# Kernel optimization log

Measured on AMD Instinct MI355X. Metric: run time of the kernel, lower is better.

Reference implementation:

```python
import jax, jax.numpy as jnp
import numpy as np

G, T, P, M = 512, 25, 10, 5
E = 32          # config.embedding_size
D0 = 2 * E      # initial node embedding dim (h_0)
HID = 32        # signed SAGE output dim
H = 128         # lstm_hidden_size
NE = 40         # edges per vote-graph per sign
N = G * T * P   # total nodes across all vote graphs
LSTM_IN = 2 * HID + 2  # 66


def _seg_mean(vals, idx, n):
    s = jax.ops.segment_sum(vals, idx, num_segments=n)
    c = jax.ops.segment_sum(jnp.ones((idx.shape[0], 1), vals.dtype), idx, num_segments=n)
    return s / jnp.maximum(c, 1.0)


def _l2norm(x, eps=1e-12):
    return x / jnp.maximum(jnp.linalg.norm(x, axis=-1, keepdims=True), eps)


def _globalize(local):
    # local: [G, T, NE] player ids in [0, P) -> flat global node ids in [0, N)
    off = (jnp.arange(G * T, dtype=local.dtype) * P).reshape(G, T, 1)
    return (local + off).reshape(-1)


def _forward(x0, add_info, Wb_pos, bb_pos, Wb_neg, bb_neg,
             Wd_pos, bd_pos, Wd_neg, bd_neg,
             W_ih, W_hh, b_ih, b_hh, hx0, cx0, Wf, bf,
             pos_src, pos_dst, neg_src, neg_dst):
    x = x0.reshape(N, D0)
    pr, pc = _globalize(pos_src), _globalize(pos_dst)
    nr, nc = _globalize(neg_src), _globalize(neg_dst)

    # base signed SAGE: cat(mean of neighbors, self) @ W + b, l2-normalized
    hp = _l2norm(jnp.concatenate([_seg_mean(x[pc], pr, N), x], -1) @ Wb_pos + bb_pos)
    hn = _l2norm(jnp.concatenate([_seg_mean(x[nc], nr, N), x], -1) @ Wb_neg + bb_neg)

    for l in range(2):  # layer_num - 1 deep layers
        app_in = _seg_mean(hp[pc], pr, N)
        app_out = _seg_mean(hp[pr], pc, N)
        ann_in = _seg_mean(hn[nc], nr, N)
        ann_out = _seg_mean(hn[nr], nc, N)
        anp_in = _seg_mean(hn[pc], pr, N)  # neg embeddings over pos edges
        apn_in = _seg_mean(hp[nc], nr, N)  # pos embeddings over neg edges
        feats_p = jnp.concatenate([app_in, app_out, ann_in, ann_out, anp_in, hp, hn], -1)
        feats_n = jnp.concatenate([ann_in, ann_out, app_in, app_out, apn_in, hn, hp], -1)
        hp_new = _l2norm(feats_p @ Wd_pos[l] + bd_pos[l])
        hn = _l2norm(feats_n @ Wd_neg[l] + bd_neg[l])
        hp = hp_new

    # per-vote embedding: cat(h_pos, h_neg, add_info)
    emb = jnp.concatenate([hp, hn], -1).reshape(G, T, P, 2 * HID)
    add_rep = jnp.repeat(add_info, T // M, axis=1)   # [G, T, P, 2]
    seq = jnp.concatenate([emb, add_rep], -1)         # [G, T, P, 66]
    seq = seq.transpose(1, 0, 2, 3).reshape(T, G * P, LSTM_IN)

    # one distinct LSTMCell per timestep (cell_num = 25)
    def step(carry, inp):
        h, c = carry
        x_t, wih, whh, bih, bhh = inp
        gates = x_t @ wih.T + bih + h @ whh.T + bhh
        i, f, g, o = jnp.split(gates, 4, axis=-1)
        c = jax.nn.sigmoid(f) * c + jax.nn.sigmoid(i) * jnp.tanh(g)
        h = jax.nn.sigmoid(o) * jnp.tanh(c)
        return (h, c), None

    (h_last, _), _ = jax.lax.scan(
        step, (hx0.reshape(G * P, H), cx0.reshape(G * P, H)),
        (seq, W_ih, W_hh, b_ih, b_hh))
    return (h_last @ Wf + bf).reshape(G, P, E)


def setup_inputs() -> dict:
    key = jax.random.key(0)
    ks = jax.random.split(key, 24)
    s = 0.1  # weight scale to keep activations/gates in a sane range
    return {
        "x0": jax.random.normal(ks[0], (G, T, P, D0), jnp.float32),
        "add_info": jax.random.uniform(ks[1], (G, M, P, 2), jnp.float32),
        "Wb_pos": jax.random.normal(ks[2], (2 * D0, HID), jnp.float32) * s,
        "bb_pos": jnp.zeros((HID,), jnp.float32),
        "Wb_neg": jax.random.normal(ks[3], (2 * D0, HID), jnp.float32) * s,
        "bb_neg": jnp.zeros((HID,), jnp.float32),
        "Wd_pos": jax.random.normal(ks[4], (2, 7 * HID, HID), jnp.float32) * s,
        "bd_pos": jnp.zeros((2, HID), jnp.float32),
        "Wd_neg": jax.random.normal(ks[5], (2, 7 * HID, HID), jnp.float32) * s,
        "bd_neg": jnp.zeros((2, HID), jnp.float32),
        "W_ih": jax.random.normal(ks[6], (T, 4 * H, LSTM_IN), jnp.float32) * s,
        "W_hh": jax.random.normal(ks[7], (T, 4 * H, H), jnp.float32) * s,
        "b_ih": jnp.zeros((T, 4 * H), jnp.float32),
        "b_hh": jnp.zeros((T, 4 * H), jnp.float32),
        "hx0": jax.random.uniform(ks[8], (G, P, H), jnp.float32),
        "cx0": jax.random.uniform(ks[9], (G, P, H), jnp.float32),
        "Wf": jax.random.normal(ks[10], (H, E), jnp.float32) * s,
        "bf": jnp.zeros((E,), jnp.float32),
        "pos_src": jax.random.randint(ks[11], (G, T, NE), 0, P, jnp.int32),
        "pos_dst": jax.random.randint(ks[12], (G, T, NE), 0, P, jnp.int32),
        "neg_src": jax.random.randint(ks[13], (G, T, NE), 0, P, jnp.int32),
        "neg_dst": jax.random.randint(ks[14], (G, T, NE), 0, P, jnp.int32),
    }


def reference(x0, add_info, Wb_pos, bb_pos, Wb_neg, bb_neg, Wd_pos, bd_pos,
              Wd_neg, bd_neg, W_ih, W_hh, b_ih, b_hh, hx0, cx0, Wf, bf,
              pos_src, pos_dst, neg_src, neg_dst):
    return _forward(x0, add_info, Wb_pos, bb_pos, Wb_neg, bb_neg,
                    Wd_pos, bd_pos, Wd_neg, bd_neg,
                    W_ih, W_hh, b_ih, b_hh, hx0, cx0, Wf, bf,
                    pos_src, pos_dst, neg_src, neg_dst)
```

## Files before the change

### kernel.cpp

```cpp
#include <hip/hip_runtime.h>
#include <math.h>

#define GG 512
#define TT 25
#define PP 10
#define MM 5
#define EE 32
#define HID 32
#define HH 128
#define NEDGE 40
#define NGRAPH (GG*TT)
#define NTOT (GG*TT*PP)

typedef __attribute__((ext_vector_type(8))) short short8v;
typedef __attribute__((ext_vector_type(4))) short short4v;
typedef __attribute__((ext_vector_type(4))) float f32x4;

#define AIDX(s,ki,mt,l) (((((s)*6+(ki))*2+(mt))*64+(l))*8)
#define WB_PER_T 196608

#define AXI(sp,mt,ki) ((((sp)*5+(mt))*2+(ki))*512)
#define AHI(sp,wh,mt) ((((sp)*2+(wh))*5+(mt))*512)
#define NWG 73728

#define MFMA16(a,b,c) __builtin_amdgcn_mfma_f32_16x16x32_bf16(a,b,c,0,0,0)

__device__ __forceinline__ unsigned short f2bf(float x){
    unsigned u = __float_as_uint(x);
    u += 0x7fffu + ((u >> 16) & 1u);
    return (unsigned short)(u >> 16);
}
__device__ __forceinline__ float bf2f(unsigned short s){
    return __uint_as_float(((unsigned)s) << 16);
}
__device__ __forceinline__ float sigm(float x){ return 1.f/(1.f+__expf(-x)); }
__device__ __forceinline__ float tanh_fast(float x){
    float ax = fabsf(x);
    float e  = __expf(-2.f*ax);
    float t  = (1.f-e)/(1.f+e);
    return copysignf(t, x);
}

__global__ void prep_kernel(const float* __restrict__ W_ih, const float* __restrict__ W_hh,
                            const float* __restrict__ b_ih, const float* __restrict__ b_hh,
                            const float* __restrict__ Wb_pos, const float* __restrict__ Wb_neg,
                            const float* __restrict__ Wd_pos, const float* __restrict__ Wd_neg,
                            short* __restrict__ wB, float* __restrict__ wadd,
                            float* __restrict__ bsum, short* __restrict__ wG)
{
    const int NW = TT*WB_PER_T;
    const int NA = TT*2*512;
    const int NB = TT*512;
    const int total = NW + NA + NB + NWG;
    for (int idx = blockIdx.x*blockDim.x + threadIdx.x; idx < total;
         idx += gridDim.x*blockDim.x) {
        if (idx < NW) {
            int e  = idx & 7;
            int l  = (idx >> 3) & 63;
            int nt = (idx >> 9) & 31;
            int rest = idx >> 14;
            int ki = rest % 6; rest /= 6;
            int s  = rest & 1;
            int t  = rest >> 1;
            int k  = ki*32 + (l >> 4)*8 + e;
            int n  = nt*16 + (l & 15);
            float wv = (k < 128) ? W_hh[(size_t)(t*512 + n)*128 + k]
                                 : W_ih[(size_t)(t*512 + n)*66 + (k - 128)];
            unsigned short hi = f2bf(wv);
            unsigned short outv = (s == 0) ? hi : f2bf(wv - bf2f(hi));
            wB[idx] = (short)outv;
        } else if (idx < NW + NA) {
            int i2 = idx - NW;
            int t = i2 / 1024, r = i2 % 1024;
            int cc = r >> 9, n = r & 511;
            wadd[i2] = W_ih[(size_t)(t*512 + n)*66 + 64 + cc];
        } else if (idx < NW + NA + NB) {
            int i3 = idx - NW - NA;
            bsum[i3] = b_ih[i3] + b_hh[i3];
        } else {
            int i4 = idx - NW - NA - NB;
            int e  = i4 & 7;
            int ll = (i4 >> 3) & 63;
            int nt = (i4 >> 9) & 1;
            int sp = (i4 >> 10) & 1;
            int u  = i4 >> 11;
            int n  = nt*16 + (ll & 15);
            int krow = (ll >> 4)*8 + e;
            float wv;
            if (u < 8) {
                int sgn = u >> 2, prod = (u >> 1) & 1, ki = u & 1;
                const float* Wb = sgn ? Wb_neg : Wb_pos;
                wv = Wb[(prod*64 + ki*32 + krow)*32 + n];
            } else {
                int v = u - 8;
                int wid = v % 7, sgn = (v / 7) & 1, lyr = v / 14;
                const float* Wd = (sgn ? Wd_neg : Wd_pos) + lyr*7168;
                wv = Wd[(wid*32 + krow)*32 + n];
            }
            unsigned short hi = f2bf(wv);
            wG[i4] = (sp == 0) ? (short)hi : (short)f2bf(wv - bf2f(hi));
        }
    }
}

__global__ __launch_bounds__(256) void graph_kernel(
    const float* __restrict__ x0,
    const float* __restrict__ bb_pos, const float* __restrict__ bb_neg,
    const float* __restrict__ bd_pos, const float* __restrict__ bd_neg,
    const short* __restrict__ wG,
    const int* __restrict__ pos_src, const int* __restrict__ pos_dst,
    const int* __restrict__ neg_src, const int* __restrict__ neg_dst,
    float* __restrict__ emb)
{
    __shared__ short U[10240];
    __shared__ float Yf[5760];
    __shared__ float Adj[8][4][10][10];

    const int tid = threadIdx.x;
    const int w   = tid >> 6;
    const int l   = tid & 63;
    const int li  = l & 15;
    const int lk  = l >> 4;
    const int s   = tid >> 7;
    const int rg  = (tid >> 3) & 15;
    const int c4  = tid & 7;
    const int gq  = rg >> 1;
    const int nbase = (rg & 1)*5;

    for (int i = tid; i < 1280; i += 256) {
        int row = i >> 4, kq = i & 15;
        float4 f = ((const float4*)x0)[(size_t)blockIdx.x*1280 + i];
        int k0 = kq*4;
        int ln = (row & 15) + 16*((k0 >> 3) & 3);
        int ki = k0 >> 5, e0 = k0 & 7, mt = row >> 4;
        float vv[4] = {f.x, f.y, f.z, f.w};
        short4v hi4, lo4;
#pragma unroll
        for (int e2 = 0; e2 < 4; ++e2) {
            unsigned short h2 = f2bf(vv[e2]);
            hi4[e2] = (short)h2;
            lo4[e2] = (short)f2bf(vv[e2] - bf2f(h2));
        }
        *(short4v*)&U[AXI(0,mt,ki) + ln*8 + e0] = hi4;
        *(short4v*)&U[AXI(1,mt,ki) + ln*8 + e0] = lo4;
    }

    int*   Ses  = (int*)Yf;
    float* Cm   = Yf + 1280;
    float* Scnt = Yf + 2880;
    for (int i = tid; i < 1280; i += 256) {
        int g = i / 160, r = i % 160, b = r / 40, e = r % 40;
        const int* p = (b==0)?pos_src:(b==1)?pos_dst:(b==2)?neg_src:neg_dst;
        Ses[i] = p[(blockIdx.x*8 + g)*40 + e];
    }
    for (int i = tid; i < 1600; i += 256) Cm[i] = 0.f;
    __syncthreads();
    for (int i = tid; i < 640; i += 256) {
        int g = i / 80, r = i % 80, si = r / 40, e = r % 40;
        int src = Ses[g*160 + (2*si)*40 + e];
        int dst = Ses[g*160 + (2*si+1)*40 + e];
        atomicAdd(&Cm[(g*2 + si)*100 + src*10 + dst], 1.f);
    }
    __syncthreads();
    for (int i = tid; i < 320; i += 256) {
        int g = i / 40, r = i % 40, b = r / 10, n = r % 10;
        int si = b >> 1, isCol = b & 1;
        float ssum = 0.f;
        for (int m = 0; m < 10; ++m)
            ssum += isCol ? Cm[(g*2+si)*100 + m*10 + n] : Cm[(g*2+si)*100 + n*10 + m];
        Scnt[i] = fmaxf(ssum, 1.f);
    }
    __syncthreads();
    for (int i = tid; i < 3200; i += 256) {
        int g = i / 400, r = i % 400, a = r / 100, rr = r % 100;
        int n = rr / 10, m = rr % 10;
        int si = a >> 1, isOut = a & 1;
        float cv = isOut ? Cm[(g*2+si)*100 + m*10 + n] : Cm[(g*2+si)*100 + n*10 + m];
        Adj[g][a][n][m] = cv / Scnt[g*40 + a*10 + n];
    }
    __syncthreads();

    f32x4 acc2[5];

    {
        const float* bb = s ? bb_neg : bb_pos;
        f32x4 b4 = *(const f32x4*)(bb + c4*4);
#pragma unroll
        for (int jj = 0; jj < 5; ++jj) acc2[jj] = b4;
    }
    for (int prod = 0; prod < 2; ++prod) {
        for (int i = 0; i < 5; ++i) {
            int jid = w*5 + i;
            int sgn = (jid >= 10);
            int rem = jid - 10*sgn;
            int nt  = (rem >= 5);
            int mt2 = rem - 5*nt;
            f32x4 cf = {0.f, 0.f, 0.f, 0.f};
            for (int ki = 0; ki < 2; ++ki) {
                short8v ah = *(const short8v*)&U[AXI(0,mt2,ki) + l*8];
                short8v al = *(const short8v*)&U[AXI(1,mt2,ki) + l*8];
                int u = sgn*4 + prod*2 + ki;
                const short* wp = wG + ((((size_t)u*2 + 0)*2 + nt)*64 + l)*8;
                short8v bh = *(const short8v*)wp;
                short8v bl = *(const short8v*)(wp + 1024);
                cf = MFMA16(ah, bh, cf);
                cf = MFMA16(ah, bl, cf);
                cf = MFMA16(al, bh, cf);
            }
#pragma unroll
            for (int r = 0; r < 4; ++r)
                Yf[(sgn*80 + mt2*16 + lk*4 + r)*36 + nt*16 + li] = cf[r];
        }
        __syncthreads();
        if (prod == 0) {
            int a = 2*s;
            for (int m = 0; m < 10; ++m) {
                f32x4 y = *(const f32x4*)&Yf[(s*80 + gq*10 + m)*36 + c4*4];
#pragma unroll
                for (int jj = 0; jj < 5; ++jj)
                    acc2[jj] += Adj[gq][a][nbase+jj][m] * y;
            }
        } else {
#pragma unroll
            for (int jj = 0; jj < 5; ++jj)
                acc2[jj] += *(const f32x4*)&Yf[(s*80 + rg*5 + jj)*36 + c4*4];
        }
        __syncthreads();
    }
#pragma unroll
    for (int jj = 0; jj < 5; ++jj) {
        f32x4 v = acc2[jj];
        float ss = v[0]*v[0] + v[1]*v[1] + v[2]*v[2] + v[3]*v[3];
        ss += __shfl_xor(ss,1); ss += __shfl_xor(ss,2); ss += __shfl_xor(ss,4);
        float rn = 1.f / fmaxf(sqrtf(ss), 1e-12f);
        v *= rn;
        int row = rg*5 + jj;
        int mt2 = row >> 4;
        int k0 = c4*4;
        int ln = (row & 15) + 16*((k0 >> 3) & 3);
        float vv[4] = {v[0], v[1], v[2], v[3]};
        short4v hi4, lo4;
#pragma unroll
        for (int e2 = 0; e2 < 4; ++e2) {
            unsigned short h2 = f2bf(vv[e2]);
            hi4[e2] = (short)h2;
            lo4[e2] = (short)f2bf(vv[e2] - bf2f(h2));
        }
        *(short4v*)&U[AHI(0,s,mt2) + ln*8 + (k0 & 7)] = hi4;
        *(short4v*)&U[AHI(1,s,mt2) + ln*8 + (k0 & 7)] = lo4;
    }
    __syncthreads();

    for (int lyr = 0; lyr < 2; ++lyr) {
        {
            const float* bd = (s ? bd_neg : bd_pos) + lyr*32;
            f32x4 b4 = *(const f32x4*)(bd + c4*4);
#pragma unroll
            for (int jj = 0; jj < 5; ++jj) acc2[jj] = b4;
        }
        for (int b = 0; b < 5; ++b) {
            const int np   = (b == 0 || b == 4) ? 2 : 1;
            const int rel0 = (b == 2 || b == 3) ? 1 : 0;
            const int wid0 = (b == 4) ? 5 : b;
            for (int i = 0; i < 5; ++i) {
                int jid = w*5 + i;
                int sgn = (jid >= 10);
                int rem = jid - 10*sgn;
                int nt  = (rem >= 5);
                int mt2 = rem - 5*nt;
                f32x4 cf = {0.f, 0.f, 0.f, 0.f};
                {
                    int wh = sgn ^ rel0;
                    int u = 8 + (lyr*2 + sgn)*7 + wid0;
                    short8v ah = *(const short8v*)&U[AHI(0,wh,mt2) + l*8];
                    short8v al = *(const short8v*)&U[AHI(1,wh,mt2) + l*8];
                    const short* wp = wG + ((((size_t)u*2 + 0)*2 + nt)*64 + l)*8;
                    short8v bh = *(const short8v*)wp;
                    short8v bl = *(const short8v*)(wp + 1024);
                    cf = MFMA16(ah, bh, cf);
                    cf = MFMA16(ah, bl, cf);
                    cf = MFMA16(al, bh, cf);
                }
                if (np == 2) {
                    int wid1 = (b == 0) ? 4 : 6;
                    int wh = sgn ^ 1;
                    int u = 8 + (lyr*2 + sgn)*7 + wid1;
                    short8v ah = *(const short8v*)&U[AHI(0,wh,mt2) + l*8];
                    short8v al = *(const short8v*)&U[AHI(1,wh,mt2) + l*8];
                    const short* wp = wG + ((((size_t)u*2 + 0)*2 + nt)*64 + l)*8;
                    short8v bh = *(const short8v*)wp;
                    short8v bl = *(const short8v*)(wp + 1024);
                    cf = MFMA16(ah, bh, cf);
                    cf = MFMA16(ah, bl, cf);
                    cf = MFMA16(al, bh, cf);
                }
#pragma unroll
                for (int r = 0; r < 4; ++r)
                    Yf[(sgn*80 + mt2*16 + lk*4 + r)*36 + nt*16 + li] = cf[r];
            }
            __syncthreads();
            if (b < 4) {
                int a = (b == 0) ? 2*s : (b == 1) ? 2*s + 1 : (b == 2) ? 2 - 2*s : 3 - 2*s;
                for (int m = 0; m < 10; ++m) {
                    f32x4 y = *(const f32x4*)&Yf[(s*80 + gq*10 + m)*36 + c4*4];
#pragma unroll
                    for (int jj = 0; jj < 5; ++jj)
                        acc2[jj] += Adj[gq][a][nbase+jj][m] * y;
                }
            } else {
#pragma unroll
                for (int jj = 0; jj < 5; ++jj)
                    acc2[jj] += *(const f32x4*)&Yf[(s*80 + rg*5 + jj)*36 + c4*4];
            }
            __syncthreads();
        }
#pragma unroll
        for (int jj = 0; jj < 5; ++jj) {
            f32x4 v = acc2[jj];
            float ss = v[0]*v[0] + v[1]*v[1] + v[2]*v[2] + v[3]*v[3];
            ss += __shfl_xor(ss,1); ss += __shfl_xor(ss,2); ss += __shfl_xor(ss,4);
            float rn = 1.f / fmaxf(sqrtf(ss), 1e-12f);
            v *= rn;
            int row = rg*5 + jj;
            if (lyr == 0) {
                int mt2 = row >> 4;
                int k0 = c4*4;
                int ln = (row & 15) + 16*((k0 >> 3) & 3);
                float vv[4] = {v[0], v[1], v[2], v[3]};
                short4v hi4, lo4;
#pragma unroll
                for (int e2 = 0; e2 < 4; ++e2) {
                    unsigned short h2 = f2bf(vv[e2]);
                    hi4[e2] = (short)h2;
                    lo4[e2] = (short)f2bf(vv[e2] - bf2f(h2));
                }
                *(short4v*)&U[AHI(0,s,mt2) + ln*8 + (k0 & 7)] = hi4;
                *(short4v*)&U[AHI(1,s,mt2) + ln*8 + (k0 & 7)] = lo4;
            } else {
                *(f32x4*)&emb[((size_t)(blockIdx.x*80 + row))*64 + s*32 + c4*4] = v;
            }
        }
        __syncthreads();
    }
}

#define LOADB(pt, pki, BH, BL)                                                 \
    {                                                                          \
        const short* wtp = wB + (size_t)(pt) * WB_PER_T;                       \
        _Pragma("unroll")                                                      \
        for (int g = 0; g < 4; ++g) {                                          \
            int nt = w + 8*g;                                                  \
            BH[g] = *(const short8v*)(wtp + (((size_t)(pki)*32 + nt)*64 + l)*8);      \
            BL[g] = *(const short8v*)(wtp + (((size_t)(6+(pki))*32 + nt)*64 + l)*8);  \
        }                                                                      \
    }

#define KI_STEP(ki, CH, CL, pt, pki, PH, PL)                                   \
    {                                                                          \
        short8v ah0 = *(const short8v*)&aP[AIDX(0,ki,0,l)];                    \
        short8v ah1 = *(const short8v*)&aP[AIDX(0,ki,1,l)];                    \
        short8v al0 = *(const short8v*)&aP[AIDX(1,ki,0,l)];                    \
        short8v al1 = *(const short8v*)&aP[AIDX(1,ki,1,l)];                    \
        LOADB(pt, pki, PH, PL)                                                 \
        _Pragma("unroll")                                                      \
        for (int g = 0; g < 4; ++g) {                                          \
            acc[0][g] = MFMA16(ah0, CH[g], acc[0][g]);                         \
            acc[0][g] = MFMA16(ah0, CL[g], acc[0][g]);                         \
            acc[0][g] = MFMA16(al0, CH[g], acc[0][g]);                         \
            acc[1][g] = MFMA16(ah1, CH[g], acc[1][g]);                         \
            acc[1][g] = MFMA16(ah1, CL[g], acc[1][g]);                         \
            acc[1][g] = MFMA16(al1, CH[g], acc[1][g]);                         \
        }                                                                      \
    }

__global__ __launch_bounds__(512) void lstm_mfma(
    const float* __restrict__ emb, const float* __restrict__ add_info,
    const short* __restrict__ wB, const float* __restrict__ wadd,
    const float* __restrict__ bsum, const float* __restrict__ hx0,
    const float* __restrict__ cx0, float* __restrict__ hbuf)
{
    __shared__ short aP[12288];
    __shared__ float Sadd[2][32][2];
    const int tid = threadIdx.x;
    const int w  = tid >> 6;
    const int l  = tid & 63;
    const int li = l & 15;
    const int lk = l >> 4;
    const int R0 = blockIdx.x * 32;

    {
        int row = tid >> 4, j0 = (tid & 15) * 8;
        const float* hp = hx0 + (size_t)(R0 + row)*128 + j0;
        float4 h0 = *(const float4*)hp;
        float4 h1 = *(const float4*)(hp + 4);
        float v[8] = {h0.x,h0.y,h0.z,h0.w,h1.x,h1.y,h1.z,h1.w};
        short8v hi, lo;
#pragma unroll
        for (int e = 0; e < 8; ++e) {
            unsigned short hs = f2bf(v[e]);
            hi[e] = (short)hs;
            lo[e] = (short)f2bf(v[e] - bf2f(hs));
        }
        int mt = row >> 4, ln = (row & 15) + 16*((j0 >> 3) & 3), ki = j0 >> 5;
        *(short8v*)&aP[AIDX(0,ki,mt,ln)] = hi;
        *(short8v*)&aP[AIDX(1,ki,mt,ln)] = lo;
    }
    {
        int row = tid >> 4, d0 = (tid & 15)*4;
        int R = R0 + row, g = R/10, p = R - 10*g;
        float4 f = *(const float4*)&emb[((size_t)(g*TT + 0)*PP + p)*64 + d0];
        int k0 = 128 + d0;
        int mt = row>>4, ln = (row&15) + 16*((k0>>3)&3), ki = k0>>5, e0 = k0&7;
        float v[4] = {f.x,f.y,f.z,f.w};
        short4v hi, lo;
#pragma unroll
        for (int e = 0; e < 4; ++e) {
            unsigned short hs = f2bf(v[e]);
            hi[e] = (short)hs;
            lo[e] = (short)f2bf(v[e] - bf2f(hs));
        }
        *(short4v*)&aP[AIDX(0,ki,mt,ln)+e0] = hi;
        *(short4v*)&aP[AIDX(1,ki,mt,ln)+e0] = lo;
    }
    if (tid < 64) {
        int row = tid >> 1, cc = tid & 1;
        int R = R0 + row, g = R/10, p = R - 10*g;
        Sadd[0][row][cc] = add_info[((size_t)(g*MM + 0)*PP + p)*2 + cc];
    }
    float c[2][4];
#pragma unroll
    for (int mt = 0; mt < 2; ++mt)
#pragma unroll
        for (int r = 0; r < 4; ++r) {
            int row = mt*16 + lk*4 + r;
            c[mt][r] = cx0[(size_t)(R0+row)*128 + 16*w + li];
        }

    short8v b0h[4], b0l[4], b1h[4], b1l[4], b2h[4], b2l[4];
    LOADB(0, 0, b0h, b0l)
    LOADB(0, 1, b1h, b1l)
    __syncthreads();

    for (int t = 0; t < TT; ++t) {
        const int tn = (t < TT-1) ? t+1 : t;
        float4 fnext;
        {
            int row = tid >> 4, d0 = (tid & 15)*4;
            int R = R0 + row, g = R/10, p = R - 10*g;
            fnext = *(const float4*)&emb[((size_t)(g*TT + tn)*PP + p)*64 + d0];
        }
        float adn0 = 0.f, adn1 = 0.f;
        if (tid < 64) {
            int rw = tid >> 1, cc = tid & 1;
            int R2 = R0 + rw, g2 = R2/10, p2 = R2 - 10*g2;
            adn0 = add_info[((size_t)(g2*MM + tn/MM)*PP + p2)*2 + cc];
            (void)adn1;
        }
        float wa0[4], wa1[4];
#pragma unroll
        for (int g = 0; g < 4; ++g) {
            wa0[g] = wadd[(size_t)(t*2+0)*512 + 128*g + 16*w + li];
            wa1[g] = wadd[(size_t)(t*2+1)*512 + 128*g + 16*w + li];
        }

        f32x4 acc[2][4];
#pragma unroll
        for (int g = 0; g < 4; ++g) {
            float bs = bsum[t*512 + 128*g + 16*w + li];
            acc[0][g] = (f32x4){bs,bs,bs,bs};
            acc[1][g] = (f32x4){bs,bs,bs,bs};
        }

        KI_STEP(0, b0h, b0l, t,  2, b2h, b2l)
        KI_STEP(1, b1h, b1l, t,  3, b0h, b0l)
        KI_STEP(2, b2h, b2l, t,  4, b1h, b1l)
        KI_STEP(3, b0h, b0l, t,  5, b2h, b2l)
        KI_STEP(4, b1h, b1l, tn, 0, b0h, b0l)
        KI_STEP(5, b2h, b2l, tn, 1, b1h, b1l)
        __syncthreads();

        const int sb = t & 1;
        const int j  = 16*w + li;
        const int jsh = 16*((j >> 3) & 3);
        const int jki = j >> 5;
        const int je  = j & 7;
#pragma unroll
        for (int mt = 0; mt < 2; ++mt) {
#pragma unroll
            for (int r = 0; r < 4; ++r) {
                int row = mt*16 + lk*4 + r;
                float ad0 = Sadd[sb][row][0], ad1 = Sadd[sb][row][1];
                float v0 = acc[mt][0][r] + ad0*wa0[0] + ad1*wa1[0];
                float v1 = acc[mt][1][r] + ad0*wa0[1] + ad1*wa1[1];
                float v2 = acc[mt][2][r] + ad0*wa0[2] + ad1*wa1[2];
                float v3 = acc[mt][3][r] + ad0*wa0[3] + ad1*wa1[3];
                float iv = sigm(v0);
                float fv = sigm(v1);
                float gv = tanh_fast(v2);
                float ov = sigm(v3);
                float cn = fv*c[mt][r] + iv*gv;
                c[mt][r] = cn;
                float hv = ov*tanh_fast(cn);
                unsigned short hs = f2bf(hv);
                int ln = (row & 15) + jsh;
                aP[AIDX(0, jki, mt, ln) + je] = (short)hs;
                aP[AIDX(1, jki, mt, ln) + je] = (short)f2bf(hv - bf2f(hs));
                if (t == TT-1) hbuf[(size_t)(R0+row)*128 + j] = hv;
            }
        }
        if (t < TT-1) {
            int row = tid >> 4, d0 = (tid & 15)*4;
            int k0 = 128 + d0;
            int mt = row>>4, ln = (row&15) + 16*((k0>>3)&3), ki = k0>>5, e0 = k0&7;
            float v[4] = {fnext.x, fnext.y, fnext.z, fnext.w};
            short4v hi, lo;
#pragma unroll
            for (int e = 0; e < 4; ++e) {
                unsigned short hs = f2bf(v[e]);
                hi[e] = (short)hs;
                lo[e] = (short)f2bf(v[e] - bf2f(hs));
            }
            *(short4v*)&aP[AIDX(0,ki,mt,ln)+e0] = hi;
            *(short4v*)&aP[AIDX(1,ki,mt,ln)+e0] = lo;
            if (tid < 64) {
                int rw = tid >> 1, cc = tid & 1;
                Sadd[sb^1][rw][cc] = adn0;
            }
        }
        __syncthreads();
    }
}

__global__ __launch_bounds__(256) void final_proj(
    const float* __restrict__ hbuf, const float* __restrict__ Wf,
    const float* __restrict__ bf, float* __restrict__ out)
{
    __shared__ float wl[128*32];
    __shared__ float hl[64][128];
    const int tid = threadIdx.x;
    const int row0 = blockIdx.x * 64;
    for (int i = tid; i < 4096; i += 256) wl[i] = Wf[i];
    for (int i = tid; i < 8192; i += 256) hl[i>>7][i&127] = hbuf[row0*128 + i];
    __syncthreads();
    const int e  = tid & 31;
    const int rg = tid >> 5;
    float b = bf[e];
    float acc[8];
#pragma unroll
    for (int r=0;r<8;++r) acc[r] = b;
    for (int k = 0; k < 128; ++k) {
        float ww = wl[k*32 + e];
#pragma unroll
        for (int r=0;r<8;++r) acc[r] += hl[rg*8+r][k]*ww;
    }
#pragma unroll
    for (int r=0;r<8;++r) out[(row0 + rg*8 + r)*32 + e] = acc[r];
}

extern "C" void kernel_launch(void* const* d_in, const int* in_sizes, int n_in,
                              void* d_out, int out_size, void* d_ws, size_t ws_size,
                              hipStream_t stream)
{
    const float* x0       = (const float*)d_in[0];
    const float* add_info = (const float*)d_in[1];
    const float* Wb_pos   = (const float*)d_in[2];
    const float* bb_pos   = (const float*)d_in[3];
    const float* Wb_neg   = (const float*)d_in[4];
    const float* bb_neg   = (const float*)d_in[5];
    const float* Wd_pos   = (const float*)d_in[6];
    const float* bd_pos   = (const float*)d_in[7];
    const float* Wd_neg   = (const float*)d_in[8];
    const float* bd_neg   = (const float*)d_in[9];
    const float* W_ih     = (const float*)d_in[10];
    const float* W_hh     = (const float*)d_in[11];
    const float* b_ih     = (const float*)d_in[12];
    const float* b_hh     = (const float*)d_in[13];
    const float* hx0      = (const float*)d_in[14];
    const float* cx0      = (const float*)d_in[15];
    const float* Wf       = (const float*)d_in[16];
    const float* bf       = (const float*)d_in[17];
    const int*   pos_src  = (const int*)d_in[18];
    const int*   pos_dst  = (const int*)d_in[19];
    const int*   neg_src  = (const int*)d_in[20];
    const int*   neg_dst  = (const int*)d_in[21];

    float* ws    = (float*)d_ws;
    float* emb   = ws;
    float* hbuf  = emb   + 8192000;
    float* bsumw = hbuf  + 655360;
    float* waddw = bsumw + 12800;
    short* wBw   = (short*)(waddw + 25600);
    short* wGw   = wBw + 4915200;

    hipLaunchKernelGGL(prep_kernel, dim3(2048), dim3(256), 0, stream,
                       W_ih, W_hh, b_ih, b_hh, Wb_pos, Wb_neg, Wd_pos, Wd_neg,
                       wBw, waddw, bsumw, wGw);
    hipLaunchKernelGGL(graph_kernel, dim3(NGRAPH/8), dim3(256), 0, stream,
                       x0, bb_pos, bb_neg, bd_pos, bd_neg, wGw,
                       pos_src, pos_dst, neg_src, neg_dst, emb);
    hipLaunchKernelGGL(lstm_mfma, dim3(160), dim3(512), 0, stream,
                       emb, add_info, wBw, waddw, bsumw, hx0, cx0, hbuf);
    hipLaunchKernelGGL(final_proj, dim3(80), dim3(256), 0, stream,
                       hbuf, Wf, bf, (float*)d_out);
}
```

Baseline: 397.7 us.

## Double-buffer Yf and overlap bucket MFMAs with adjacency aggregation in graph kernel

The shared Yf staging buffer is doubled so the MFMA products for the next bucket can be computed and stored while the previous bucket's adjacency aggregation reads the other buffer. This cuts the number of block-wide barriers per layer from two per bucket to roughly one. Loops are fully unrolled through macros. The cost is extra shared memory, which may reduce occupancy, and more live registers for the two sets of MFMA accumulators.

```diff
diff --git a/kernel.cpp b/kernel.cpp
--- a/kernel.cpp
+++ b/kernel.cpp
@@ -113,7 +113,7 @@
     float* __restrict__ emb)
 {
     __shared__ short U[10240];
-    __shared__ float Yf[5760];
+    __shared__ float Yf[2][5760];
     __shared__ float Adj[8][4][10][10];
 
     const int tid = threadIdx.x;
@@ -145,9 +145,9 @@
         *(short4v*)&U[AXI(1,mt,ki) + ln*8 + e0] = lo4;
     }
 
-    int*   Ses  = (int*)Yf;
-    float* Cm   = Yf + 1280;
-    float* Scnt = Yf + 2880;
+    int*   Ses  = (int*)&Yf[0][0];
+    float* Cm   = &Yf[0][0] + 1280;
+    float* Scnt = &Yf[0][0] + 2880;
     for (int i = tid; i < 1280; i += 256) {
         int g = i / 160, r = i % 160, b = r / 40, e = r % 40;
         const int* p = (b==0)?pos_src:(b==1)?pos_dst:(b==2)?neg_src:neg_dst;
@@ -180,7 +180,93 @@
     }
     __syncthreads();
 
+#define JDECOMP(i) \
+        int jid = w*5 + (i); \
+        int sgn = (jid >= 10); \
+        int rem = jid - 10*sgn; \
+        int nt  = (rem >= 5); \
+        int mt2 = rem - 5*nt;
+
+#define BASE_BUCKET(prod, CF) \
+    _Pragma("unroll") \
+    for (int i = 0; i < 5; ++i) { \
+        JDECOMP(i) \
+        f32x4 cf = {0.f,0.f,0.f,0.f}; \
+        _Pragma("unroll") \
+        for (int ki = 0; ki < 2; ++ki) { \
+            short8v ah = *(const short8v*)&U[AXI(0,mt2,ki) + l*8]; \
+            short8v al = *(const short8v*)&U[AXI(1,mt2,ki) + l*8]; \
+            int u = sgn*4 + (prod)*2 + ki; \
+            const short* wp = wG + ((((size_t)u*2)*2 + nt)*64 + l)*8; \
+            short8v bh = *(const short8v*)wp; \
+            short8v bl = *(const short8v*)(wp + 1024); \
+            cf = MFMA16(ah, bh, cf); \
+            cf = MFMA16(ah, bl, cf); \
+            cf = MFMA16(al, bh, cf); \
+        } \
+        CF[i] = cf; \
+    }
+
+#define DEEP_BUCKET(lyr, q, CF) \
+    _Pragma("unroll") \
+    for (int i = 0; i < 5; ++i) { \
+        JDECOMP(i) \
+        f32x4 cf = {0.f,0.f,0.f,0.f}; \
+        { \
+            const int wid0 = ((q) == 4) ? 5 : (q); \
+            const int rel0 = ((q) == 2 || (q) == 3) ? 1 : 0; \
+            int wh = sgn ^ rel0; \
+            int u = 8 + ((lyr)*2 + sgn)*7 + wid0; \
+            short8v ah = *(const short8v*)&U[AHI(0,wh,mt2) + l*8]; \
+            short8v al = *(const short8v*)&U[AHI(1,wh,mt2) + l*8]; \
+            const short* wp = wG + ((((size_t)u*2)*2 + nt)*64 + l)*8; \
+            short8v bh = *(const short8v*)wp; \
+            short8v bl = *(const short8v*)(wp + 1024); \
+            cf = MFMA16(ah, bh, cf); \
+            cf = MFMA16(ah, bl, cf); \
+            cf = MFMA16(al, bh, cf); \
+        } \
+        if ((q) == 0 || (q) == 4) { \
+            const int wid1 = ((q) == 0) ? 4 : 6; \
+            int wh = sgn ^ 1; \
+            int u = 8 + ((lyr)*2 + sgn)*7 + wid1; \
+            short8v ah = *(const short8v*)&U[AHI(0,wh,mt2) + l*8]; \
+            short8v al = *(const short8v*)&U[AHI(1,wh,mt2) + l*8]; \
+            const short* wp = wG + ((((size_t)u*2)*2 + nt)*64 + l)*8; \
+            short8v bh = *(const short8v*)wp; \
+            short8v bl = *(const short8v*)(wp + 1024); \
+            cf = MFMA16(ah, bh, cf); \
+            cf = MFMA16(ah, bl, cf); \
+            cf = MFMA16(al, bh, cf); \
+        } \
+        CF[i] = cf; \
+    }
+
+#define STORE_CF(CF, buf) \
+    _Pragma("unroll") \
+    for (int i = 0; i < 5; ++i) { \
+        JDECOMP(i) \
+        _Pragma("unroll") \
+        for (int r = 0; r < 4; ++r) \
+            Yf[buf][(sgn*80 + mt2*16 + lk*4 + r)*36 + nt*16 + li] = CF[i][r]; \
+    }
+
+#define APPLY_ADJ(aIdx, buf) \
+    _Pragma("unroll") \
+    for (int m = 0; m < 10; ++m) { \
+        f32x4 y = *(const f32x4*)&Yf[buf][(s*80 + gq*10 + m)*36 + c4*4]; \
+        _Pragma("unroll") \
+        for (int jj = 0; jj < 5; ++jj) \
+            acc2[jj] += Adj[gq][aIdx][nbase+jj][m] * y; \
+    }
+
+#define APPLY_SELF(buf) \
+    _Pragma("unroll") \
+    for (int jj = 0; jj < 5; ++jj) \
+        acc2[jj] += *(const f32x4*)&Yf[buf][(s*80 + rg*5 + jj)*36 + c4*4];
+
     f32x4 acc2[5];
+    f32x4 cfA[5], cfB[5];
 
     {
         const float* bb = s ? bb_neg : bb_pos;
@@ -188,45 +274,14 @@
 #pragma unroll
         for (int jj = 0; jj < 5; ++jj) acc2[jj] = b4;
     }
-    for (int prod = 0; prod < 2; ++prod) {
-        for (int i = 0; i < 5; ++i) {
-            int jid = w*5 + i;
-            int sgn = (jid >= 10);
-            int rem = jid - 10*sgn;
-            int nt  = (rem >= 5);
-            int mt2 = rem - 5*nt;
-            f32x4 cf = {0.f, 0.f, 0.f, 0.f};
-            for (int ki = 0; ki < 2; ++ki) {
-                short8v ah = *(const short8v*)&U[AXI(0,mt2,ki) + l*8];
-                short8v al = *(const short8v*)&U[AXI(1,mt2,ki) + l*8];
-                int u = sgn*4 + prod*2 + ki;
-                const short* wp = wG + ((((size_t)u*2 + 0)*2 + nt)*64 + l)*8;
-                short8v bh = *(const short8v*)wp;
-                short8v bl = *(const short8v*)(wp + 1024);
-                cf = MFMA16(ah, bh, cf);
-                cf = MFMA16(ah, bl, cf);
-                cf = MFMA16(al, bh, cf);
-            }
-#pragma unroll
-            for (int r = 0; r < 4; ++r)
-                Yf[(sgn*80 + mt2*16 + lk*4 + r)*36 + nt*16 + li] = cf[r];
-        }
-        __syncthreads();
-        if (prod == 0) {
-            int a = 2*s;
-            for (int m = 0; m < 10; ++m) {
-                f32x4 y = *(const f32x4*)&Yf[(s*80 + gq*10 + m)*36 + c4*4];
-#pragma unroll
-                for (int jj = 0; jj < 5; ++jj)
-                    acc2[jj] += Adj[gq][a][nbase+jj][m] * y;
-            }
-        } else {
-#pragma unroll
-            for (int jj = 0; jj < 5; ++jj)
-                acc2[jj] += *(const f32x4*)&Yf[(s*80 + rg*5 + jj)*36 + c4*4];
-        }
-        __syncthreads();
-    }
+    BASE_BUCKET(0, cfA)
+    STORE_CF(cfA, 0)
+    BASE_BUCKET(1, cfB)
+    __syncthreads();
+    APPLY_ADJ(2*s, 0)
+    STORE_CF(cfB, 1)
+    __syncthreads();
+    APPLY_SELF(1)
 #pragma unroll
     for (int jj = 0; jj < 5; ++jj) {
         f32x4 v = acc2[jj];
@@ -258,62 +313,26 @@
 #pragma unroll
             for (int jj = 0; jj < 5; ++jj) acc2[jj] = b4;
         }
-        for (int b = 0; b < 5; ++b) {
-            const int np   = (b == 0 || b == 4) ? 2 : 1;
-            const int rel0 = (b == 2 || b == 3) ? 1 : 0;
-            const int wid0 = (b == 4) ? 5 : b;
-            for (int i = 0; i < 5; ++i) {
-                int jid = w*5 + i;
-                int sgn = (jid >= 10);
-                int rem = jid - 10*sgn;
-                int nt  = (rem >= 5);
-                int mt2 = rem - 5*nt;
-                f32x4 cf = {0.f, 0.f, 0.f, 0.f};
-                {
-                    int wh = sgn ^ rel0;
-                    int u = 8 + (lyr*2 + sgn)*7 + wid0;
-                    short8v ah = *(const short8v*)&U[AHI(0,wh,mt2) + l*8];
-                    short8v al = *(const short8v*)&U[AHI(1,wh,mt2) + l*8];
-                    const short* wp = wG + ((((size_t)u*2 + 0)*2 + nt)*64 + l)*8;
-                    short8v bh = *(const short8v*)wp;
-                    short8v bl = *(const short8v*)(wp + 1024);
-                    cf = MFMA16(ah, bh, cf);
-                    cf = MFMA16(ah, bl, cf);
-                    cf = MFMA16(al, bh, cf);
-                }
-                if (np == 2) {
-                    int wid1 = (b == 0) ? 4 : 6;
-                    int wh = sgn ^ 1;
-                    int u = 8 + (lyr*2 + sgn)*7 + wid1;
-                    short8v ah = *(const short8v*)&U[AHI(0,wh,mt2) + l*8];
-                    short8v al = *(const short8v*)&U[AHI(1,wh,mt2) + l*8];
-                    const short* wp = wG + ((((size_t)u*2 + 0)*2 + nt)*64 + l)*8;
-                    short8v bh = *(const short8v*)wp;
-                    short8v bl = *(const short8v*)(wp + 1024);
-                    cf = MFMA16(ah, bh, cf);
-                    cf = MFMA16(ah, bl, cf);
-                    cf = MFMA16(al, bh, cf);
-                }
-#pragma unroll
-                for (int r = 0; r < 4; ++r)
-                    Yf[(sgn*80 + mt2*16 + lk*4 + r)*36 + nt*16 + li] = cf[r];
-            }
-            __syncthreads();
-            if (b < 4) {
-                int a = (b == 0) ? 2*s : (b == 1) ? 2*s + 1 : (b == 2) ? 2 - 2*s : 3 - 2*s;
-                for (int m = 0; m < 10; ++m) {
-                    f32x4 y = *(const f32x4*)&Yf[(s*80 + gq*10 + m)*36 + c4*4];
-#pragma unroll
-                    for (int jj = 0; jj < 5; ++jj)
-                        acc2[jj] += Adj[gq][a][nbase+jj][m] * y;
-                }
-            } else {
-#pragma unroll
-                for (int jj = 0; jj < 5; ++jj)
-                    acc2[jj] += *(const f32x4*)&Yf[(s*80 + rg*5 + jj)*36 + c4*4];
-            }
-            __syncthreads();
-        }
+        DEEP_BUCKET(lyr, 0, cfA)
+        STORE_CF(cfA, 0)
+        DEEP_BUCKET(lyr, 1, cfB)
+        __syncthreads();
+        APPLY_ADJ(2*s, 0)
+        STORE_CF(cfB, 1)
+        DEEP_BUCKET(lyr, 2, cfA)
+        __syncthreads();
+        APPLY_ADJ(2*s+1, 1)
+        STORE_CF(cfA, 0)
+        DEEP_BUCKET(lyr, 3, cfB)
+        __syncthreads();
+        APPLY_ADJ(2-2*s, 0)
+        STORE_CF(cfB, 1)
+        DEEP_BUCKET(lyr, 4, cfA)
+        __syncthreads();
+        APPLY_ADJ(3-2*s, 1)
+        STORE_CF(cfA, 0)
+        __syncthreads();
+        APPLY_SELF(0)
 #pragma unroll
         for (int jj = 0; jj < 5; ++jj) {
             f32x4 v = acc2[jj];
@@ -449,12 +468,11 @@
             int R = R0 + row, g = R/10, p = R - 10*g;
             fnext = *(const float4*)&emb[((size_t)(g*TT + tn)*PP + p)*64 + d0];
         }
-        float adn0 = 0.f, adn1 = 0.f;
+        float adn0 = 0.f;
         if (tid < 64) {
             int rw = tid >> 1, cc = tid & 1;
             int R2 = R0 + rw, g2 = R2/10, p2 = R2 - 10*g2;
             adn0 = add_info[((size_t)(g2*MM + tn/MM)*PP + p2)*2 + cc];
-            (void)adn1;
         }
         float wa0[4], wa1[4];
 #pragma unroll
```

Result: faster. 378.1 us (-4.9%).

## Double-buffer Yf staging to overlap MFMA products with adjacency aggregation

Applied to the files above, without the earlier changes.

The Yf shared staging buffer becomes double-buffered. Each stage's MFMA results are held in registers, and while those are computed the previous stage's buffer is aggregated through the adjacency, which cuts the barriers per stage from two to roughly one. This trades extra LDS (about 23 KB more) and more live registers for less barrier stalling, and may lower occupancy of graph_kernel.

```diff
diff --git a/kernel.cpp b/kernel.cpp
--- a/kernel.cpp
+++ b/kernel.cpp
@@ -113,7 +113,7 @@
     float* __restrict__ emb)
 {
     __shared__ short U[10240];
-    __shared__ float Yf[5760];
+    __shared__ float Yf[2][5760];
     __shared__ float Adj[8][4][10][10];
 
     const int tid = threadIdx.x;
@@ -145,9 +145,9 @@
         *(short4v*)&U[AXI(1,mt,ki) + ln*8 + e0] = lo4;
     }
 
-    int*   Ses  = (int*)Yf;
-    float* Cm   = Yf + 1280;
-    float* Scnt = Yf + 2880;
+    int*   Ses  = (int*)&Yf[0][0];
+    float* Cm   = &Yf[0][0] + 1280;
+    float* Scnt = &Yf[0][0] + 2880;
     for (int i = tid; i < 1280; i += 256) {
         int g = i / 160, r = i % 160, b = r / 40, e = r % 40;
         const int* p = (b==0)?pos_src:(b==1)?pos_dst:(b==2)?neg_src:neg_dst;
@@ -181,52 +181,75 @@
     __syncthreads();
 
     f32x4 acc2[5];
-
-    {
-        const float* bb = s ? bb_neg : bb_pos;
-        f32x4 b4 = *(const f32x4*)(bb + c4*4);
-#pragma unroll
-        for (int jj = 0; jj < 5; ++jj) acc2[jj] = b4;
-    }
-    for (int prod = 0; prod < 2; ++prod) {
+    f32x4 cf[5];
+
+    auto store_cf = [&](int buf) {
+#pragma unroll
         for (int i = 0; i < 5; ++i) {
             int jid = w*5 + i;
             int sgn = (jid >= 10);
             int rem = jid - 10*sgn;
             int nt  = (rem >= 5);
             int mt2 = rem - 5*nt;
-            f32x4 cf = {0.f, 0.f, 0.f, 0.f};
+#pragma unroll
+            for (int r = 0; r < 4; ++r)
+                Yf[buf][(sgn*80 + mt2*16 + lk*4 + r)*36 + nt*16 + li] = cf[i][r];
+        }
+    };
+    auto apply_adj = [&](int aIdx, int buf) {
+#pragma unroll
+        for (int m = 0; m < 10; ++m) {
+            f32x4 y = *(const f32x4*)&Yf[buf][(s*80 + gq*10 + m)*36 + c4*4];
+#pragma unroll
+            for (int jj = 0; jj < 5; ++jj)
+                acc2[jj] += Adj[gq][aIdx][nbase+jj][m] * y;
+        }
+    };
+    auto apply_self = [&](int buf) {
+#pragma unroll
+        for (int jj = 0; jj < 5; ++jj)
+            acc2[jj] += *(const f32x4*)&Yf[buf][(s*80 + rg*5 + jj)*36 + c4*4];
+    };
+
+    {
+        const float* bb = s ? bb_neg : bb_pos;
+        f32x4 b4 = *(const f32x4*)(bb + c4*4);
+#pragma unroll
+        for (int jj = 0; jj < 5; ++jj) acc2[jj] = b4;
+    }
+    for (int prod = 0; prod < 2; ++prod) {
+#pragma unroll
+        for (int i = 0; i < 5; ++i) {
+            int jid = w*5 + i;
+            int sgn = (jid >= 10);
+            int rem = jid - 10*sgn;
+            int nt  = (rem >= 5);
+            int mt2 = rem - 5*nt;
+            f32x4 c0 = {0.f,0.f,0.f,0.f};
+#pragma unroll
             for (int ki = 0; ki < 2; ++ki) {
                 short8v ah = *(const short8v*)&U[AXI(0,mt2,ki) + l*8];
                 short8v al = *(const short8v*)&U[AXI(1,mt2,ki) + l*8];
                 int u = sgn*4 + prod*2 + ki;
-                const short* wp = wG + ((((size_t)u*2 + 0)*2 + nt)*64 + l)*8;
+                const short* wp = wG + ((((size_t)u*2)*2 + nt)*64 + l)*8;
                 short8v bh = *(const short8v*)wp;
                 short8v bl = *(const short8v*)(wp + 1024);
-                cf = MFMA16(ah, bh, cf);
-                cf = MFMA16(ah, bl, cf);
-                cf = MFMA16(al, bh, cf);
-            }
-#pragma unroll
-            for (int r = 0; r < 4; ++r)
-                Yf[(sgn*80 + mt2*16 + lk*4 + r)*36 + nt*16 + li] = cf[r];
-        }
-        __syncthreads();
+                c0 = MFMA16(ah, bh, c0);
+                c0 = MFMA16(ah, bl, c0);
+                c0 = MFMA16(al, bh, c0);
+            }
+            cf[i] = c0;
+        }
         if (prod == 0) {
-            int a = 2*s;
-            for (int m = 0; m < 10; ++m) {
-                f32x4 y = *(const f32x4*)&Yf[(s*80 + gq*10 + m)*36 + c4*4];
-#pragma unroll
-                for (int jj = 0; jj < 5; ++jj)
-                    acc2[jj] += Adj[gq][a][nbase+jj][m] * y;
-            }
+            store_cf(0);
         } else {
-#pragma unroll
-            for (int jj = 0; jj < 5; ++jj)
-                acc2[jj] += *(const f32x4*)&Yf[(s*80 + rg*5 + jj)*36 + c4*4];
-        }
-        __syncthreads();
-    }
+            __syncthreads();
+            apply_adj(2*s, 0);
+            store_cf(1);
+        }
+    }
+    __syncthreads();
+    apply_self(1);
 #pragma unroll
     for (int jj = 0; jj < 5; ++jj) {
         f32x4 v = acc2[jj];
@@ -258,62 +281,56 @@
 #pragma unroll
             for (int jj = 0; jj < 5; ++jj) acc2[jj] = b4;
         }
-        for (int b = 0; b < 5; ++b) {
-            const int np   = (b == 0 || b == 4) ? 2 : 1;
-            const int rel0 = (b == 2 || b == 3) ? 1 : 0;
-            const int wid0 = (b == 4) ? 5 : b;
+        for (int q = 0; q <= 4; ++q) {
+            const int wid0 = (q == 4) ? 5 : q;
+            const int rel0 = (q == 2 || q == 3) ? 1 : 0;
+            const int two  = (q == 0 || q == 4);
+            const int wid1 = (q == 0) ? 4 : 6;
+#pragma unroll
             for (int i = 0; i < 5; ++i) {
                 int jid = w*5 + i;
                 int sgn = (jid >= 10);
                 int rem = jid - 10*sgn;
                 int nt  = (rem >= 5);
                 int mt2 = rem - 5*nt;
-                f32x4 cf = {0.f, 0.f, 0.f, 0.f};
+                f32x4 c0 = {0.f,0.f,0.f,0.f};
                 {
                     int wh = sgn ^ rel0;
                     int u = 8 + (lyr*2 + sgn)*7 + wid0;
                     short8v ah = *(const short8v*)&U[AHI(0,wh,mt2) + l*8];
                     short8v al = *(const short8v*)&U[AHI(1,wh,mt2) + l*8];
-                    const short* wp = wG + ((((size_t)u*2 + 0)*2 + nt)*64 + l)*8;
+                    const short* wp = wG + ((((size_t)u*2)*2 + nt)*64 + l)*8;
                     short8v bh = *(const short8v*)wp;
                     short8v bl = *(const short8v*)(wp + 1024);
-                    cf = MFMA16(ah, bh, cf);
-                    cf = MFMA16(ah, bl, cf);
-                    cf = MFMA16(al, bh, cf);
+                    c0 = MFMA16(ah, bh, c0);
+                    c0 = MFMA16(ah, bl, c0);
+                    c0 = MFMA16(al, bh, c0);
                 }
-                if (np == 2) {
-                    int wid1 = (b == 0) ? 4 : 6;
+                if (two) {
                     int wh = sgn ^ 1;
                     int u = 8 + (lyr*2 + sgn)*7 + wid1;
                     short8v ah = *(const short8v*)&U[AHI(0,wh,mt2) + l*8];
                     short8v al = *(const short8v*)&U[AHI(1,wh,mt2) + l*8];
-                    const short* wp = wG + ((((size_t)u*2 + 0)*2 + nt)*64 + l)*8;
+                    const short* wp = wG + ((((size_t)u*2)*2 + nt)*64 + l)*8;
                     short8v bh = *(const short8v*)wp;
                     short8v bl = *(const short8v*)(wp + 1024);
-                    cf = MFMA16(ah, bh, cf);
-                    cf = MFMA16(ah, bl, cf);
-                    cf = MFMA16(al, bh, cf);
+                    c0 = MFMA16(ah, bh, c0);
+                    c0 = MFMA16(ah, bl, c0);
+                    c0 = MFMA16(al, bh, c0);
                 }
-#pragma unroll
-                for (int r = 0; r < 4; ++r)
-                    Yf[(sgn*80 + mt2*16 + lk*4 + r)*36 + nt*16 + li] = cf[r];
-            }
-            __syncthreads();
-            if (b < 4) {
-                int a = (b == 0) ? 2*s : (b == 1) ? 2*s + 1 : (b == 2) ? 2 - 2*s : 3 - 2*s;
-                for (int m = 0; m < 10; ++m) {
-                    f32x4 y = *(const f32x4*)&Yf[(s*80 + gq*10 + m)*36 + c4*4];
-#pragma unroll
-                    for (int jj = 0; jj < 5; ++jj)
-                        acc2[jj] += Adj[gq][a][nbase+jj][m] * y;
-                }
-            } else {
-#pragma unroll
-                for (int jj = 0; jj < 5; ++jj)
-                    acc2[jj] += *(const f32x4*)&Yf[(s*80 + rg*5 + jj)*36 + c4*4];
-            }
-            __syncthreads();
-        }
+                cf[i] = c0;
+            }
+            if (q > 0) {
+                __syncthreads();
+                int qq = q - 1;
+                int aIdx = (qq == 0) ? 2*s : (qq == 1) ? 2*s + 1
+                         : (qq == 2) ? 2 - 2*s : 3 - 2*s;
+                apply_adj(aIdx, qq & 1);
+            }
+            store_cf(q & 1);
+        }
+        __syncthreads();
+        apply_self(0);
 #pragma unroll
         for (int jj = 0; jj < 5; ++jj) {
             f32x4 v = acc2[jj];
@@ -449,12 +466,11 @@
             int R = R0 + row, g = R/10, p = R - 10*g;
             fnext = *(const float4*)&emb[((size_t)(g*TT + tn)*PP + p)*64 + d0];
         }
-        float adn0 = 0.f, adn1 = 0.f;
+        float adn0 = 0.f;
         if (tid < 64) {
             int rw = tid >> 1, cc = tid & 1;
             int R2 = R0 + rw, g2 = R2/10, p2 = R2 - 10*g2;
             adn0 = add_info[((size_t)(g2*MM + tn/MM)*PP + p2)*2 + cc];
-            (void)adn1;
         }
         float wa0[4], wa1[4];
 #pragma unroll
```

Measured after the change: 380.2 us (median of 2 runs). 4.4% less time.
